# Performance work log

Hardware: AMD Instinct MI355X
Metric: run time of the kernel (lower is better)

## Reference

```python
import jax, jax.numpy as jnp
import numpy as np

BS, H, L, D = 16, 16, 4096, 32  # bs, n_heads, seq_len(=q_len), head_dim

def setup_inputs() -> dict:
    key = jax.random.key(0)
    kq, kk, kv = jax.random.split(key, 3)
    q = jax.random.normal(kq, (BS, H, L, D), dtype=jnp.float32)
    k = jax.random.normal(kk, (BS, H, D, L), dtype=jnp.float32)
    v = jax.random.normal(kv, (BS, H, L, D), dtype=jnp.float32)
    return {"q": q, "k": k, "v": v}

def reference(q, k, v):
    # reordered attention: scores = (k @ v) / sqrt(seq_len) -> [bs,h,d_k,d_v]
    seq_len = v.shape[2]
    scores = jnp.einsum('bhds,bhse->bhde', k, v) / jnp.sqrt(jnp.float32(seq_len))
    # faithful to source: softmax over dim=0 (the batch dimension)
    attn_weights = jax.nn.softmax(scores, axis=0)
    # dropout p=0.0 -> identity
    # output = q @ weights -> [bs,h,q_len,d_v]
    output = jnp.einsum('bhld,bhde->bhle', q, attn_weights)
    return output, attn_weights
```

## Files before the change

kernel.cpp:

```cpp
#include <hip/hip_runtime.h>

#define BS 16
#define NH 16
#define LQ 4096
#define DH 32

constexpr int SPLIT = 8;
constexpr int SCHUNK = LQ / SPLIT;
constexpr size_t OUT_ELEMS = (size_t)BS * NH * LQ * DH;
constexpr int HDE = NH * DH * DH;

__global__ __launch_bounds__(256, 2) void kv_partial(const float* __restrict__ k,
                                                     const float* __restrict__ v,
                                                     float* __restrict__ part) {
    __shared__ float lds[4 * 4096];
    const int tid  = threadIdx.x;
    const int wid  = tid >> 6;
    const int lane = tid & 63;
    const int blk  = blockIdx.x;
    const int p    = blk & (SPLIT - 1);
    const int bh   = blk >> 3;

    float* kt = &lds[wid * 4096];
    float* vt = kt + 2048;

    const int d0 = (lane >> 3) << 2;
    const int e0 = (lane & 7) << 2;

    const float* kb = k + (size_t)bh * DH * LQ;
    const float* vb = v + (size_t)bh * LQ * DH;

    const int s_base = p * SCHUNK + wid * 128;
    const int krow = lane >> 4;
    const int c    = lane & 15;
    const int kcol = c << 2;

    float4 kr[2][8], vr[2][8];
#pragma unroll
    for (int st = 0; st < 2; ++st) {
        const int s0 = s_base + st * 64;
#pragma unroll
        for (int i = 0; i < 8; ++i)
            kr[st][i] = *(const float4*)(kb + (size_t)(krow + 4 * i) * LQ + s0 + kcol);
#pragma unroll
        for (int i = 0; i < 8; ++i)
            vr[st][i] = *(const float4*)(vb + (size_t)s0 * DH + ((lane + 64 * i) << 2));
    }

    float4 acc0 = {0,0,0,0}, acc1 = {0,0,0,0}, acc2 = {0,0,0,0}, acc3 = {0,0,0,0};

    const int wsw = (c & 7) << 2;

#pragma unroll
    for (int st = 0; st < 2; ++st) {
        asm volatile("s_waitcnt lgkmcnt(0)" ::: "memory");
#pragma unroll
        for (int i = 0; i < 8; ++i) {
            const int rsw = (krow + 4 * i) ^ wsw;
            kt[(kcol + 0) * 32 + rsw] = kr[st][i].x;
            kt[(kcol + 1) * 32 + rsw] = kr[st][i].y;
            kt[(kcol + 2) * 32 + rsw] = kr[st][i].z;
            kt[(kcol + 3) * 32 + rsw] = kr[st][i].w;
        }
#pragma unroll
        for (int i = 0; i < 8; ++i)
            *(float4*)(vt + ((lane + 64 * i) << 2)) = vr[st][i];

#pragma unroll 8
        for (int s = 0; s < 64; ++s) {
            const int sw = ((s >> 2) & 7) << 2;
            const float4 kv = *(const float4*)(kt + s * 32 + (d0 ^ sw));
            const float4 vv = *(const float4*)(vt + s * 32 + e0);
            acc0.x = fmaf(kv.x, vv.x, acc0.x);
            acc0.y = fmaf(kv.x, vv.y, acc0.y);
            acc0.z = fmaf(kv.x, vv.z, acc0.z);
            acc0.w = fmaf(kv.x, vv.w, acc0.w);
            acc1.x = fmaf(kv.y, vv.x, acc1.x);
            acc1.y = fmaf(kv.y, vv.y, acc1.y);
            acc1.z = fmaf(kv.y, vv.z, acc1.z);
            acc1.w = fmaf(kv.y, vv.w, acc1.w);
            acc2.x = fmaf(kv.z, vv.x, acc2.x);
            acc2.y = fmaf(kv.z, vv.y, acc2.y);
            acc2.z = fmaf(kv.z, vv.z, acc2.z);
            acc2.w = fmaf(kv.z, vv.w, acc2.w);
            acc3.x = fmaf(kv.w, vv.x, acc3.x);
            acc3.y = fmaf(kv.w, vv.y, acc3.y);
            acc3.z = fmaf(kv.w, vv.z, acc3.z);
            acc3.w = fmaf(kv.w, vv.w, acc3.w);
        }
    }

    asm volatile("s_waitcnt lgkmcnt(0)" ::: "memory");
    *(float4*)(kt + (d0 + 0) * 32 + e0) = acc0;
    *(float4*)(kt + (d0 + 1) * 32 + e0) = acc1;
    *(float4*)(kt + (d0 + 2) * 32 + e0) = acc2;
    *(float4*)(kt + (d0 + 3) * 32 + e0) = acc3;
    __syncthreads();

    float4 s0 = *(const float4*)(&lds[0 * 4096] + tid * 4);
    float4 s1 = *(const float4*)(&lds[1 * 4096] + tid * 4);
    float4 s2 = *(const float4*)(&lds[2 * 4096] + tid * 4);
    float4 s3 = *(const float4*)(&lds[3 * 4096] + tid * 4);
    float4 r;
    r.x = (s0.x + s1.x) + (s2.x + s3.x);
    r.y = (s0.y + s1.y) + (s2.y + s3.y);
    r.z = (s0.z + s1.z) + (s2.z + s3.z);
    r.w = (s0.w + s1.w) + (s2.w + s3.w);
    *(float4*)(part + ((size_t)p * (BS * NH) + bh) * 1024 + tid * 4) = r;
}

__global__ __launch_bounds__(256) void softmax_b(const float* __restrict__ part,
                                                 float* __restrict__ wts) {
    int idx = blockIdx.x * 256 + threadIdx.x;

    float sc[BS];
#pragma unroll
    for (int b = 0; b < BS; ++b) {
        float s = 0.f;
#pragma unroll
        for (int p = 0; p < SPLIT; ++p) {
            s += part[(((size_t)p * BS * NH + (size_t)b * NH) << 10) + idx];
        }
        sc[b] = s * (1.0f / 64.0f);
    }

    float m = sc[0];
#pragma unroll
    for (int b = 1; b < BS; ++b) m = fmaxf(m, sc[b]);
    float sum = 0.f;
#pragma unroll
    for (int b = 0; b < BS; ++b) { sc[b] = __expf(sc[b] - m); sum += sc[b]; }
    float inv = 1.0f / sum;
#pragma unroll
    for (int b = 0; b < BS; ++b) {
        wts[(size_t)b * HDE + idx] = sc[b] * inv;
    }
}

__global__ __launch_bounds__(256, 2) void qw(const float* __restrict__ q,
                                             const float* __restrict__ wts,
                                             float* __restrict__ out) {
    __shared__ float qs[128 * 36];
    const int blk = blockIdx.x;
    const int bh  = blk >> 5;
    const int lt  = blk & 31;
    const int tid = threadIdx.x;

    const float* qbase = q + ((size_t)bh * LQ + lt * 128) * DH;

#pragma unroll
    for (int pp = 0; pp < 4; ++pp) {
        const int idx = pp * 256 + tid;
        const int row = idx >> 3;
        const int c4  = idx & 7;
        const float4 t = *(const float4*)(qbase + idx * 4);
        *(float4*)(qs + row * 36 + c4 * 4) = t;
    }

    const int lsub = tid >> 3;
    const int e0   = (tid & 7) << 2;

    float4 Wf[32];
    const float* wbase = wts + (size_t)bh * (DH * DH) + e0;
#pragma unroll
    for (int d = 0; d < 32; ++d) Wf[d] = *(const float4*)(wbase + d * DH);

    __syncthreads();

    float* obase = out + ((size_t)bh * LQ + lt * 128) * DH;

#pragma unroll
    for (int r = 0; r < 4; ++r) {
        const int lr = lsub + r * 32;
        const float* qrow = qs + lr * 36;
        float4 acc = {0,0,0,0};
#pragma unroll
        for (int d4 = 0; d4 < 32; d4 += 4) {
            const float4 qv = *(const float4*)(qrow + d4);
            acc.x = fmaf(qv.x, Wf[d4 + 0].x, acc.x);
            acc.x = fmaf(qv.y, Wf[d4 + 1].x, acc.x);
            acc.x = fmaf(qv.z, Wf[d4 + 2].x, acc.x);
            acc.x = fmaf(qv.w, Wf[d4 + 3].x, acc.x);

            acc.y = fmaf(qv.x, Wf[d4 + 0].y, acc.y);
            acc.y = fmaf(qv.y, Wf[d4 + 1].y, acc.y);
            acc.y = fmaf(qv.z, Wf[d4 + 2].y, acc.y);
            acc.y = fmaf(qv.w, Wf[d4 + 3].y, acc.y);

            acc.z = fmaf(qv.x, Wf[d4 + 0].z, acc.z);
            acc.z = fmaf(qv.y, Wf[d4 + 1].z, acc.z);
            acc.z = fmaf(qv.z, Wf[d4 + 2].z, acc.z);
            acc.z = fmaf(qv.w, Wf[d4 + 3].z, acc.z);

            acc.w = fmaf(qv.x, Wf[d4 + 0].w, acc.w);
            acc.w = fmaf(qv.y, Wf[d4 + 1].w, acc.w);
            acc.w = fmaf(qv.z, Wf[d4 + 2].w, acc.w);
            acc.w = fmaf(qv.w, Wf[d4 + 3].w, acc.w);
        }
        *(float4*)(obase + (size_t)lr * DH + e0) = acc;
    }
}

extern "C" void kernel_launch(void* const* d_in, const int* in_sizes, int n_in,
                              void* d_out, int out_size, void* d_ws, size_t ws_size,
                              hipStream_t stream) {
    const float* q = (const float*)d_in[0];
    const float* k = (const float*)d_in[1];
    const float* v = (const float*)d_in[2];
    float* out  = (float*)d_out;
    float* wts  = out + OUT_ELEMS;
    float* part = (float*)d_ws;

    kv_partial<<<BS * NH * SPLIT, 256, 0, stream>>>(k, v, part);
    softmax_b<<<HDE / 256, 256, 0, stream>>>(part, wts);
    qw<<<BS * NH * (LQ / 128), 256, 0, stream>>>(q, wts, out);
}
```

Baseline: 159.8 us.

## Stream K/V tiles into LDS with async double-buffered global_load_lds in kv_partial

Rewrites the K·V partial-product kernel so K and V tiles are copied straight from global memory into LDS with global_load_lds, double-buffered across 8 steps of 64 sequence elements. Each wave now works on a slice of every tile instead of a private chunk, which cuts LDS use and raises the occupancy hint from 2 to 5 blocks per CU. The goal is to overlap global loads with the FMA loop and drop the register staging and transposing scatter stores. In exchange it adds a block-wide barrier every step and depends on an XOR swizzle being correct. The qw change is a cosmetic helper refactor.

```diff
diff --git a/kernel.cpp b/kernel.cpp
--- a/kernel.cpp
+++ b/kernel.cpp
@@ -10,103 +10,111 @@
 constexpr size_t OUT_ELEMS = (size_t)BS * NH * LQ * DH;
 constexpr int HDE = NH * DH * DH;
 
-__global__ __launch_bounds__(256, 2) void kv_partial(const float* __restrict__ k,
+__device__ __forceinline__ void async_cp16(float* dst, const float* src) {
+    __builtin_amdgcn_global_load_lds(
+        (const __attribute__((address_space(1))) void*)src,
+        (__attribute__((address_space(3))) void*)dst, 16, 0, 0);
+}
+
+__device__ __forceinline__ void fma4(float4& a, float s, const float4& v) {
+    a.x = fmaf(s, v.x, a.x);
+    a.y = fmaf(s, v.y, a.y);
+    a.z = fmaf(s, v.z, a.z);
+    a.w = fmaf(s, v.w, a.w);
+}
+
+__global__ __launch_bounds__(256, 5) void kv_partial(const float* __restrict__ k,
                                                      const float* __restrict__ v,
                                                      float* __restrict__ part) {
-    __shared__ float lds[4 * 4096];
+    __shared__ float lds[8192];
     const int tid  = threadIdx.x;
     const int wid  = tid >> 6;
     const int lane = tid & 63;
-    const int blk  = blockIdx.x;
-    const int p    = blk & (SPLIT - 1);
-    const int bh   = blk >> 3;
-
-    float* kt = &lds[wid * 4096];
-    float* vt = kt + 2048;
-
-    const int d0 = (lane >> 3) << 2;
-    const int e0 = (lane & 7) << 2;
+    const int p    = blockIdx.x & (SPLIT - 1);
+    const int bh   = blockIdx.x >> 3;
+
+    const int dgl = lane >> 3;
+    const int d0  = dgl << 2;
+    const int e0  = (lane & 7) << 2;
 
     const float* kb = k + (size_t)bh * DH * LQ;
     const float* vb = v + (size_t)bh * LQ * DH;
-
-    const int s_base = p * SCHUNK + wid * 128;
-    const int krow = lane >> 4;
-    const int c    = lane & 15;
-    const int kcol = c << 2;
-
-    float4 kr[2][8], vr[2][8];
-#pragma unroll
-    for (int st = 0; st < 2; ++st) {
-        const int s0 = s_base + st * 64;
-#pragma unroll
-        for (int i = 0; i < 8; ++i)
-            kr[st][i] = *(const float4*)(kb + (size_t)(krow + 4 * i) * LQ + s0 + kcol);
-#pragma unroll
-        for (int i = 0; i < 8; ++i)
-            vr[st][i] = *(const float4*)(vb + (size_t)s0 * DH + ((lane + 64 * i) << 2));
+    const int s_blk = p * SCHUNK;
+
+    const int i0 = wid << 1;
+    const int i1 = i0 + 1;
+    const size_t ksrc0 = (size_t)((i0 << 2) + (lane >> 4)) * LQ + (((lane & 15) ^ i0) << 2);
+    const size_t ksrc1 = (size_t)((i1 << 2) + (lane >> 4)) * LQ + (((lane & 15) ^ i1) << 2);
+    const int voff_l0 = (i0 << 8) + (lane << 2);
+    const int voff_l1 = (i1 << 8) + (lane << 2);
+
+    int koff[4], voff[4];
+#pragma unroll
+    for (int bi = 0; bi < 4; ++bi) {
+        const int g = (wid << 2) + bi;
+        koff[bi] = (d0 << 6) + (((g ^ dgl) & 15) << 2);
+        voff[bi] = (g << 7) + e0;
     }
 
     float4 acc0 = {0,0,0,0}, acc1 = {0,0,0,0}, acc2 = {0,0,0,0}, acc3 = {0,0,0,0};
 
-    const int wsw = (c & 7) << 2;
-
-#pragma unroll
-    for (int st = 0; st < 2; ++st) {
-        asm volatile("s_waitcnt lgkmcnt(0)" ::: "memory");
-#pragma unroll
-        for (int i = 0; i < 8; ++i) {
-            const int rsw = (krow + 4 * i) ^ wsw;
-            kt[(kcol + 0) * 32 + rsw] = kr[st][i].x;
-            kt[(kcol + 1) * 32 + rsw] = kr[st][i].y;
-            kt[(kcol + 2) * 32 + rsw] = kr[st][i].z;
-            kt[(kcol + 3) * 32 + rsw] = kr[st][i].w;
-        }
-#pragma unroll
-        for (int i = 0; i < 8; ++i)
-            *(float4*)(vt + ((lane + 64 * i) << 2)) = vr[st][i];
-
-#pragma unroll 8
-        for (int s = 0; s < 64; ++s) {
-            const int sw = ((s >> 2) & 7) << 2;
-            const float4 kv = *(const float4*)(kt + s * 32 + (d0 ^ sw));
-            const float4 vv = *(const float4*)(vt + s * 32 + e0);
-            acc0.x = fmaf(kv.x, vv.x, acc0.x);
-            acc0.y = fmaf(kv.x, vv.y, acc0.y);
-            acc0.z = fmaf(kv.x, vv.z, acc0.z);
-            acc0.w = fmaf(kv.x, vv.w, acc0.w);
-            acc1.x = fmaf(kv.y, vv.x, acc1.x);
-            acc1.y = fmaf(kv.y, vv.y, acc1.y);
-            acc1.z = fmaf(kv.y, vv.z, acc1.z);
-            acc1.w = fmaf(kv.y, vv.w, acc1.w);
-            acc2.x = fmaf(kv.z, vv.x, acc2.x);
-            acc2.y = fmaf(kv.z, vv.y, acc2.y);
-            acc2.z = fmaf(kv.z, vv.z, acc2.z);
-            acc2.w = fmaf(kv.z, vv.w, acc2.w);
-            acc3.x = fmaf(kv.w, vv.x, acc3.x);
-            acc3.y = fmaf(kv.w, vv.y, acc3.y);
-            acc3.z = fmaf(kv.w, vv.z, acc3.z);
-            acc3.w = fmaf(kv.w, vv.w, acc3.w);
-        }
-    }
-
-    asm volatile("s_waitcnt lgkmcnt(0)" ::: "memory");
-    *(float4*)(kt + (d0 + 0) * 32 + e0) = acc0;
-    *(float4*)(kt + (d0 + 1) * 32 + e0) = acc1;
-    *(float4*)(kt + (d0 + 2) * 32 + e0) = acc2;
-    *(float4*)(kt + (d0 + 3) * 32 + e0) = acc3;
+    async_cp16(lds        + (i0 << 8), kb + ksrc0 + s_blk);
+    async_cp16(lds        + (i1 << 8), kb + ksrc1 + s_blk);
+    async_cp16(lds + 4096 + (i0 << 8), vb + ((size_t)s_blk << 5) + voff_l0);
+    async_cp16(lds + 4096 + (i1 << 8), vb + ((size_t)s_blk << 5) + voff_l1);
     __syncthreads();
 
-    float4 s0 = *(const float4*)(&lds[0 * 4096] + tid * 4);
-    float4 s1 = *(const float4*)(&lds[1 * 4096] + tid * 4);
-    float4 s2 = *(const float4*)(&lds[2 * 4096] + tid * 4);
-    float4 s3 = *(const float4*)(&lds[3 * 4096] + tid * 4);
+#pragma unroll
+    for (int t = 0; t < 8; ++t) {
+        float* kc = lds +        ((t & 1) << 11);
+        float* vc = lds + 4096 + ((t & 1) << 11);
+        if (t < 7) {
+            float* kn = lds +        (((t + 1) & 1) << 11);
+            float* vn = lds + 4096 + (((t + 1) & 1) << 11);
+            const int sb = s_blk + (t + 1) * 64;
+            async_cp16(kn + (i0 << 8), kb + ksrc0 + sb);
+            async_cp16(kn + (i1 << 8), kb + ksrc1 + sb);
+            async_cp16(vn + (i0 << 8), vb + ((size_t)sb << 5) + voff_l0);
+            async_cp16(vn + (i1 << 8), vb + ((size_t)sb << 5) + voff_l1);
+        }
+
+#pragma unroll
+        for (int bi = 0; bi < 4; ++bi) {
+            const float4 kq0 = *(const float4*)(kc + koff[bi]);
+            const float4 kq1 = *(const float4*)(kc + koff[bi] + 64);
+            const float4 kq2 = *(const float4*)(kc + koff[bi] + 128);
+            const float4 kq3 = *(const float4*)(kc + koff[bi] + 192);
+            const float4 vv0 = *(const float4*)(vc + voff[bi]);
+            const float4 vv1 = *(const float4*)(vc + voff[bi] + 32);
+            const float4 vv2 = *(const float4*)(vc + voff[bi] + 64);
+            const float4 vv3 = *(const float4*)(vc + voff[bi] + 96);
+
+            fma4(acc0, kq0.x, vv0); fma4(acc0, kq0.y, vv1); fma4(acc0, kq0.z, vv2); fma4(acc0, kq0.w, vv3);
+            fma4(acc1, kq1.x, vv0); fma4(acc1, kq1.y, vv1); fma4(acc1, kq1.z, vv2); fma4(acc1, kq1.w, vv3);
+            fma4(acc2, kq2.x, vv0); fma4(acc2, kq2.y, vv1); fma4(acc2, kq2.z, vv2); fma4(acc2, kq2.w, vv3);
+            fma4(acc3, kq3.x, vv0); fma4(acc3, kq3.y, vv1); fma4(acc3, kq3.z, vv2); fma4(acc3, kq3.w, vv3);
+        }
+        __syncthreads();
+    }
+
+    float* red = lds;
+    *(float4*)(red + (wid << 10) + ((d0 + 0) << 5) + e0) = acc0;
+    *(float4*)(red + (wid << 10) + ((d0 + 1) << 5) + e0) = acc1;
+    *(float4*)(red + (wid << 10) + ((d0 + 2) << 5) + e0) = acc2;
+    *(float4*)(red + (wid << 10) + ((d0 + 3) << 5) + e0) = acc3;
+    __syncthreads();
+
+    const int t4 = tid << 2;
+    const float4 r0 = *(const float4*)(red + t4);
+    const float4 r1 = *(const float4*)(red + 1024 + t4);
+    const float4 r2 = *(const float4*)(red + 2048 + t4);
+    const float4 r3 = *(const float4*)(red + 3072 + t4);
     float4 r;
-    r.x = (s0.x + s1.x) + (s2.x + s3.x);
-    r.y = (s0.y + s1.y) + (s2.y + s3.y);
-    r.z = (s0.z + s1.z) + (s2.z + s3.z);
-    r.w = (s0.w + s1.w) + (s2.w + s3.w);
-    *(float4*)(part + ((size_t)p * (BS * NH) + bh) * 1024 + tid * 4) = r;
+    r.x = (r0.x + r1.x) + (r2.x + r3.x);
+    r.y = (r0.y + r1.y) + (r2.y + r3.y);
+    r.z = (r0.z + r1.z) + (r2.z + r3.z);
+    r.w = (r0.w + r1.w) + (r2.w + r3.w);
+    *(float4*)(part + ((size_t)p * (BS * NH) + bh) * 1024 + t4) = r;
 }
 
 __global__ __launch_bounds__(256) void softmax_b(const float* __restrict__ part,
@@ -118,8 +126,8 @@
     for (int b = 0; b < BS; ++b) {
         float s = 0.f;
 #pragma unroll
-        for (int p = 0; p < SPLIT; ++p) {
-            s += part[(((size_t)p * BS * NH + (size_t)b * NH) << 10) + idx];
+        for (int pp = 0; pp < SPLIT; ++pp) {
+            s += part[(((size_t)pp * BS * NH + (size_t)b * NH) << 10) + idx];
         }
         sc[b] = s * (1.0f / 64.0f);
     }
@@ -177,25 +185,10 @@
 #pragma unroll
         for (int d4 = 0; d4 < 32; d4 += 4) {
             const float4 qv = *(const float4*)(qrow + d4);
-            acc.x = fmaf(qv.x, Wf[d4 + 0].x, acc.x);
-            acc.x = fmaf(qv.y, Wf[d4 + 1].x, acc.x);
-            acc.x = fmaf(qv.z, Wf[d4 + 2].x, acc.x);
-            acc.x = fmaf(qv.w, Wf[d4 + 3].x, acc.x);
-
-            acc.y = fmaf(qv.x, Wf[d4 + 0].y, acc.y);
-            acc.y = fmaf(qv.y, Wf[d4 + 1].y, acc.y);
-            acc.y = fmaf(qv.z, Wf[d4 + 2].y, acc.y);
-            acc.y = fmaf(qv.w, Wf[d4 + 3].y, acc.y);
-
-            acc.z = fmaf(qv.x, Wf[d4 + 0].z, acc.z);
-            acc.z = fmaf(qv.y, Wf[d4 + 1].z, acc.z);
-            acc.z = fmaf(qv.z, Wf[d4 + 2].z, acc.z);
-            acc.z = fmaf(qv.w, Wf[d4 + 3].z, acc.z);
-
-            acc.w = fmaf(qv.x, Wf[d4 + 0].w, acc.w);
-            acc.w = fmaf(qv.y, Wf[d4 + 1].w, acc.w);
-            acc.w = fmaf(qv.z, Wf[d4 + 2].w, acc.w);
-            acc.w = fmaf(qv.w, Wf[d4 + 3].w, acc.w);
+            fma4(acc, qv.x, Wf[d4 + 0]);
+            fma4(acc, qv.y, Wf[d4 + 1]);
+            fma4(acc, qv.z, Wf[d4 + 2]);
+            fma4(acc, qv.w, Wf[d4 + 3]);
         }
         *(float4*)(obase + (size_t)lr * DH + e0) = acc;
     }
```

New measurement: 171.3 us. 7.2% more time.
